# Kernel optimization log

Measured on AMD Instinct MI355X. Metric: run time of the kernel, lower is better.

## Reference

```python
import jax, jax.numpy as jnp
import numpy as np

N, E, IN_DIM, HID = 50000, 800000, 512, 256
EPS = 1e-5


def _gat_layer(x, W, a_src, a_dst, b, src, dst, n, heads, ch):
    # x: [N, F_in] -> h: [N, H, C]
    h = (x @ W).reshape(n, heads, ch)
    alpha_src = jnp.sum(h * a_src, axis=-1)  # [N, H]
    alpha_dst = jnp.sum(h * a_dst, axis=-1)  # [N, H]
    e = jax.nn.leaky_relu(alpha_src[src] + alpha_dst[dst], negative_slope=0.2)  # [E', H]
    # segment softmax over incoming edges of each destination node
    m = jax.ops.segment_max(e, dst, num_segments=n)  # [N, H]
    ex = jnp.exp(e - m[dst])
    den = jax.ops.segment_sum(ex, dst, num_segments=n)  # [N, H]
    alpha = ex / den[dst]
    out = jax.ops.segment_sum(alpha[:, :, None] * h[src], dst, num_segments=n)  # [N, H, C]
    return out.reshape(n, heads * ch) + b


def _layer_norm(x, w, b):
    mu = jnp.mean(x, axis=-1, keepdims=True)
    var = jnp.mean(jnp.square(x - mu), axis=-1, keepdims=True)
    return (x - mu) * jax.lax.rsqrt(var + EPS) * w + b


def setup_inputs() -> dict:
    key = jax.random.key(0)
    ks = jax.random.split(key, 16)
    d = {}
    d['x'] = jax.random.normal(ks[0], (N, IN_DIM), dtype=jnp.float32)
    d['edge_index'] = jax.random.randint(ks[1], (2, E), 0, N, dtype=jnp.int32)
    s = 0.05
    # layer 0: GATConv(512, 64, heads=4)
    d['W0'] = jax.random.normal(ks[2], (IN_DIM, HID), dtype=jnp.float32) * s
    d['as0'] = jax.random.normal(ks[3], (4, 64), dtype=jnp.float32) * s
    d['ad0'] = jax.random.normal(ks[4], (4, 64), dtype=jnp.float32) * s
    d['b0'] = jnp.zeros((HID,), dtype=jnp.float32)
    d['lnw0'] = jnp.ones((HID,), dtype=jnp.float32)
    d['lnb0'] = jnp.zeros((HID,), dtype=jnp.float32)
    # layer 1: GATConv(256, 64, heads=4)
    d['W1'] = jax.random.normal(ks[5], (HID, HID), dtype=jnp.float32) * s
    d['as1'] = jax.random.normal(ks[6], (4, 64), dtype=jnp.float32) * s
    d['ad1'] = jax.random.normal(ks[7], (4, 64), dtype=jnp.float32) * s
    d['b1'] = jnp.zeros((HID,), dtype=jnp.float32)
    d['lnw1'] = jnp.ones((HID,), dtype=jnp.float32)
    d['lnb1'] = jnp.zeros((HID,), dtype=jnp.float32)
    # layer 2: GATConv(256, 256, heads=1)
    d['W2'] = jax.random.normal(ks[8], (HID, HID), dtype=jnp.float32) * s
    d['as2'] = jax.random.normal(ks[9], (1, HID), dtype=jnp.float32) * s
    d['ad2'] = jax.random.normal(ks[10], (1, HID), dtype=jnp.float32) * s
    d['b2'] = jnp.zeros((HID,), dtype=jnp.float32)
    d['lnw2'] = jnp.ones((HID,), dtype=jnp.float32)
    d['lnb2'] = jnp.zeros((HID,), dtype=jnp.float32)
    return d


def reference(x, edge_index, W0, as0, ad0, b0, lnw0, lnb0,
              W1, as1, ad1, b1, lnw1, lnb1,
              W2, as2, ad2, b2, lnw2, lnb2):
    n = x.shape[0]
    loop = jnp.arange(n, dtype=edge_index.dtype)
    src = jnp.concatenate([edge_index[0], loop])  # PyG add_self_loops=True
    dst = jnp.concatenate([edge_index[1], loop])
    h = _gat_layer(x, W0, as0, ad0, b0, src, dst, n, 4, 64)
    h = jax.nn.elu(_layer_norm(h, lnw0, lnb0))
    h = _gat_layer(h, W1, as1, ad1, b1, src, dst, n, 4, 64)
    h = jax.nn.elu(_layer_norm(h, lnw1, lnb1))
    h = _gat_layer(h, W2, as2, ad2, b2, src, dst, n, 1, HID)
    h = jax.nn.elu(_layer_norm(h, lnw2, lnb2))
    return h
```

## Files before the change

kernel.cpp:

```cpp
#include <hip/hip_runtime.h>

#define HID 256
#define EPSV 1e-5f
#define ASTR 72
#define BSTR 40

typedef __bf16 bf16x8 __attribute__((ext_vector_type(8)));
typedef float  floatx4 __attribute__((ext_vector_type(4)));

static __device__ __forceinline__ ushort f2bf(float f) {
  union { float f; unsigned int i; } c; c.f = f;
  unsigned int u = c.i;
  u += 0x7FFFu + ((u >> 16) & 1u);
  return (ushort)(u >> 16);
}
static __device__ __forceinline__ float bf2f(ushort u) {
  union { unsigned int i; float f; } c; c.i = ((unsigned int)u) << 16; return c.f;
}

__global__ void count_kernel(const int* __restrict__ ei, int* __restrict__ deg, int E, int tot) {
  int i = blockIdx.x * blockDim.x + threadIdx.x;
  if (i < tot) {
    int dst = (i < E) ? ei[E + i] : (i - E);
    atomicAdd(&deg[dst], 1);
  }
}

__global__ void scanA_kernel(const int* __restrict__ deg, int* __restrict__ incl,
                             int* __restrict__ sums, int n) {
  __shared__ int buf[1024];
  const int t = threadIdx.x;
  const int i = blockIdx.x * 1024 + t;
  int x = (i < n) ? deg[i] : 0;
  buf[t] = x;
  __syncthreads();
  for (int off = 1; off < 1024; off <<= 1) {
    int v = (t >= off) ? buf[t - off] : 0;
    __syncthreads();
    buf[t] += v;
    __syncthreads();
  }
  if (i < n) incl[i] = buf[t];
  if (t == 1023) sums[blockIdx.x] = buf[1023];
}

__global__ void scanB_kernel(int* __restrict__ sums, int* __restrict__ offs, int nblk) {
  __shared__ int buf[256];
  const int t = threadIdx.x;
  int x = (t < nblk) ? sums[t] : 0;
  buf[t] = x;
  __syncthreads();
  for (int off = 1; off < 256; off <<= 1) {
    int v = (t >= off) ? buf[t - off] : 0;
    __syncthreads();
    buf[t] += v;
    __syncthreads();
  }
  if (t < nblk) offs[t] = buf[t] - x;
  if (t == nblk) offs[nblk] = buf[nblk - 1];
}

__global__ void scanC_kernel(const int* __restrict__ deg, const int* __restrict__ incl,
                             const int* __restrict__ offs, int* __restrict__ rp,
                             int* __restrict__ cur, int n, int nblk) {
  const int i = blockIdx.x * 1024 + threadIdx.x;
  if (i < n) {
    int v = offs[blockIdx.x] + incl[i] - deg[i];
    rp[i] = v;
    cur[i] = v;
  }
  if (i == 0) rp[n] = offs[nblk];
}

__global__ void scatter_kernel(const int* __restrict__ ei, int* __restrict__ cur,
                               int* __restrict__ csr, int E, int tot) {
  int i = blockIdx.x * blockDim.x + threadIdx.x;
  if (i < tot) {
    int src = (i < E) ? ei[i] : (i - E);
    int dst = (i < E) ? ei[E + i] : (i - E);
    int pos = atomicAdd(&cur[dst], 1);
    csr[pos] = src;
  }
}

__global__ __launch_bounds__(256) void transpose_kernel(
    const float* __restrict__ W, ushort* __restrict__ Wt, int K) {
  __shared__ ushort tile[32][33];
  const int tx = threadIdx.x & 31, ty = threadIdx.x >> 5;
  const int bm = blockIdx.x * 32;
  const int bk = blockIdx.y * 32;
  #pragma unroll
  for (int yy = ty; yy < 32; yy += 8)
    tile[tx][yy] = f2bf(W[(size_t)(bk + yy) * 256 + bm + tx]);
  __syncthreads();
  #pragma unroll
  for (int yy = ty; yy < 32; yy += 8)
    Wt[(size_t)(bm + yy) * K + bk + tx] = tile[yy][tx];
}

static __device__ __forceinline__ void alpha_epilogue(
    const floatx4 (&acc)[4][4], const float* __restrict__ avs,
    const float* __restrict__ avd, float* __restrict__ asrc,
    float* __restrict__ adst, int row0, int col0, int wm, int wn,
    int quad, int m16, int nrows) {
  float sv[4], dv[4];
  #pragma unroll
  for (int j = 0; j < 4; j++) {
    int col = col0 + wn + j * 16 + m16;
    sv[j] = avs[col];
    dv[j] = avd[col];
  }
  const int idx = (col0 + wn) >> 6;
  #pragma unroll
  for (int i = 0; i < 4; i++) {
    #pragma unroll
    for (int r = 0; r < 4; r++) {
      int row = row0 + wm + i * 16 + quad * 4 + r;
      float s = 0.f, d = 0.f;
      #pragma unroll
      for (int j = 0; j < 4; j++) {
        s = fmaf(acc[i][j][r], sv[j], s);
        d = fmaf(acc[i][j][r], dv[j], d);
      }
      #pragma unroll
      for (int o = 1; o < 16; o <<= 1) { s += __shfl_xor(s, o); d += __shfl_xor(d, o); }
      if (m16 == 0 && row < nrows) {
        asrc[row * 4 + idx] = s;
        adst[row * 4 + idx] = d;
      }
    }
  }
}

__global__ __launch_bounds__(256) void gemm_kernel(
    const float* __restrict__ A, const ushort* __restrict__ Bt,
    ushort* __restrict__ hb, const float* __restrict__ avs,
    const float* __restrict__ avd, float* __restrict__ asrc,
    float* __restrict__ adst, int nrows, int K) {
  __shared__ ushort At[128 * ASTR];
  __shared__ ushort Bs[128 * BSTR];
  const int tid  = threadIdx.x;
  const int lane = tid & 63;
  const int wave = tid >> 6;
  const int quad = lane >> 4;
  const int m16  = lane & 15;
  const int row0 = blockIdx.x * 128;
  const int col0 = blockIdx.y * 128;
  const int wm = (wave >> 1) * 64;
  const int wn = (wave & 1) * 64;

  floatx4 acc[4][4];
  #pragma unroll
  for (int i = 0; i < 4; i++)
    #pragma unroll
    for (int j = 0; j < 4; j++) acc[i][j] = (floatx4){0.f, 0.f, 0.f, 0.f};

  const int arow = tid >> 3;
  const int acol = (tid & 7) * 4;
  const int brow = tid >> 2;
  const int bcol = (tid & 3) * 8;

  const float* pa[4];
  const ushort* pb[2];
  #pragma unroll
  for (int i = 0; i < 4; i++) {
    int r = arow + 32 * i;
    int ar = min(row0 + r, nrows - 1);
    pa[i] = A + (size_t)ar * K + acol;
  }
  #pragma unroll
  for (int i = 0; i < 2; i++)
    pb[i] = Bt + (size_t)(col0 + brow + 64 * i) * K + bcol;

  floatx4 rA[4];
  int4 rB[2];
  #pragma unroll
  for (int i = 0; i < 4; i++) rA[i] = *(const floatx4*)pa[i];
  #pragma unroll
  for (int i = 0; i < 2; i++) rB[i] = *(const int4*)pb[i];

  for (int k0 = 0; k0 < K; k0 += 32) {
    #pragma unroll
    for (int i = 0; i < 4; i++) {
      int r = arow + 32 * i;
      floatx4 v = rA[i];
      unsigned u0 = __float_as_uint(v[0]), u1 = __float_as_uint(v[1]);
      unsigned u2 = __float_as_uint(v[2]), u3 = __float_as_uint(v[3]);
      unsigned ph0 = __builtin_amdgcn_perm(u1, u0, 0x07060302u);
      unsigned ph1 = __builtin_amdgcn_perm(u3, u2, 0x07060302u);
      float l0 = v[0] - __uint_as_float(u0 & 0xffff0000u);
      float l1 = v[1] - __uint_as_float(u1 & 0xffff0000u);
      float l2 = v[2] - __uint_as_float(u2 & 0xffff0000u);
      float l3 = v[3] - __uint_as_float(u3 & 0xffff0000u);
      unsigned pl0 = __builtin_amdgcn_perm(__float_as_uint(l1), __float_as_uint(l0), 0x07060302u);
      unsigned pl1 = __builtin_amdgcn_perm(__float_as_uint(l3), __float_as_uint(l2), 0x07060302u);
      *(uint2*)&At[r * ASTR + acol]      = make_uint2(ph0, ph1);
      *(uint2*)&At[r * ASTR + 32 + acol] = make_uint2(pl0, pl1);
    }
    #pragma unroll
    for (int i = 0; i < 2; i++)
      *(int4*)&Bs[(brow + 64 * i) * BSTR + bcol] = rB[i];
    __syncthreads();
    if (k0 + 32 < K) {
      #pragma unroll
      for (int i = 0; i < 4; i++) rA[i] = *(const floatx4*)(pa[i] + k0 + 32);
      #pragma unroll
      for (int i = 0; i < 2; i++) rB[i] = *(const int4*)(pb[i] + k0 + 32);
    }
    bf16x8 bfr[4];
    #pragma unroll
    for (int j = 0; j < 4; j++)
      bfr[j] = *(const bf16x8*)&Bs[(wn + j * 16 + m16) * BSTR + quad * 8];
    #pragma unroll
    for (int p = 0; p < 2; p++) {
      bf16x8 af[4];
      #pragma unroll
      for (int i = 0; i < 4; i++)
        af[i] = *(const bf16x8*)&At[(wm + i * 16 + m16) * ASTR + p * 32 + quad * 8];
      #pragma unroll
      for (int i = 0; i < 4; i++)
        #pragma unroll
        for (int j = 0; j < 4; j++)
          acc[i][j] = __builtin_amdgcn_mfma_f32_16x16x32_bf16(af[i], bfr[j], acc[i][j], 0, 0, 0);
    }
    __syncthreads();
  }
  #pragma unroll
  for (int i = 0; i < 4; i++) {
    int rbase = row0 + wm + i * 16 + quad * 4;
    #pragma unroll
    for (int j = 0; j < 4; j++) {
      int col = col0 + wn + j * 16 + m16;
      #pragma unroll
      for (int r = 0; r < 4; r++) {
        int row = rbase + r;
        if (row < nrows) hb[(size_t)row * HID + col] = f2bf(acc[i][j][r]);
      }
    }
  }
  alpha_epilogue(acc, avs, avd, asrc, adst, row0, col0, wm, wn, quad, m16, nrows);
}

__global__ __launch_bounds__(256) void gemm_packed_kernel(
    const ushort* __restrict__ A, const ushort* __restrict__ Bt,
    ushort* __restrict__ hb, const float* __restrict__ avs,
    const float* __restrict__ avd, float* __restrict__ asrc,
    float* __restrict__ adst, int nrows) {
  __shared__ ushort At[128 * BSTR];
  __shared__ ushort Bs[128 * BSTR];
  const int tid  = threadIdx.x;
  const int lane = tid & 63;
  const int wave = tid >> 6;
  const int quad = lane >> 4;
  const int m16  = lane & 15;
  const int row0 = blockIdx.x * 128;
  const int col0 = blockIdx.y * 128;
  const int wm = (wave >> 1) * 64;
  const int wn = (wave & 1) * 64;

  floatx4 acc[4][4];
  #pragma unroll
  for (int i = 0; i < 4; i++)
    #pragma unroll
    for (int j = 0; j < 4; j++) acc[i][j] = (floatx4){0.f, 0.f, 0.f, 0.f};

  const int srow = tid >> 2;
  const int scol = (tid & 3) * 8;

  const ushort* pa[2];
  const ushort* pb[2];
  #pragma unroll
  for (int i = 0; i < 2; i++) {
    int r = srow + 64 * i;
    int ar = min(row0 + r, nrows - 1);
    pa[i] = A + (size_t)ar * 512 + scol;
    pb[i] = Bt + (size_t)(col0 + r) * 256 + scol;
  }

  int4 rA[2], rB[2];
  #pragma unroll
  for (int i = 0; i < 2; i++) { rA[i] = *(const int4*)pa[i]; rB[i] = *(const int4*)pb[i]; }

  for (int k0 = 0; k0 < 512; k0 += 32) {
    #pragma unroll
    for (int i = 0; i < 2; i++) {
      int r = srow + 64 * i;
      *(int4*)&At[r * BSTR + scol] = rA[i];
      *(int4*)&Bs[r * BSTR + scol] = rB[i];
    }
    __syncthreads();
    if (k0 + 32 < 512) {
      int kn = k0 + 32, kbn = kn & 255;
      #pragma unroll
      for (int i = 0; i < 2; i++) {
        rA[i] = *(const int4*)(pa[i] + kn);
        rB[i] = *(const int4*)(pb[i] + kbn);
      }
    }
    bf16x8 af[4], bfr[4];
    #pragma unroll
    for (int j = 0; j < 4; j++)
      bfr[j] = *(const bf16x8*)&Bs[(wn + j * 16 + m16) * BSTR + quad * 8];
    #pragma unroll
    for (int i = 0; i < 4; i++)
      af[i] = *(const bf16x8*)&At[(wm + i * 16 + m16) * BSTR + quad * 8];
    #pragma unroll
    for (int i = 0; i < 4; i++)
      #pragma unroll
      for (int j = 0; j < 4; j++)
        acc[i][j] = __builtin_amdgcn_mfma_f32_16x16x32_bf16(af[i], bfr[j], acc[i][j], 0, 0, 0);
    __syncthreads();
  }
  #pragma unroll
  for (int i = 0; i < 4; i++) {
    int rbase = row0 + wm + i * 16 + quad * 4;
    #pragma unroll
    for (int j = 0; j < 4; j++) {
      int col = col0 + wn + j * 16 + m16;
      #pragma unroll
      for (int r = 0; r < 4; r++) {
        int row = rbase + r;
        if (row < nrows) hb[(size_t)row * HID + col] = f2bf(acc[i][j][r]);
      }
    }
  }
  alpha_epilogue(acc, avs, avd, asrc, adst, row0, col0, wm, wn, quad, m16, nrows);
}

__global__ __launch_bounds__(256) void agg_ln_kernel(
    const ushort* __restrict__ hb, const float* __restrict__ asrc,
    const float* __restrict__ adst, const int* __restrict__ rp,
    const int* __restrict__ csr,
    const float* __restrict__ bias, const float* __restrict__ lnw,
    const float* __restrict__ lnb, ushort* __restrict__ apk,
    float* __restrict__ fout, int H, int n) {
  __shared__ float2 exs[4][64];
  const int t = threadIdx.x;
  const int w = t >> 6, lane = t & 63;
  const int nid = blockIdx.x * 4 + w;
  if (nid >= n) return;
  const int CH = (H == 4) ? 16 : 64;
  const int jj = lane & (CH - 1);
  const int hh = (H == 4) ? (lane >> 4) : 0;
  const int ch = 4 * lane;
  float ad;
  if (H == 4) {
    ad = adst[nid * 4 + hh];
  } else {
    floatx4 t4 = *(const floatx4*)(adst + nid * 4);
    ad = t4[0] + t4[1] + t4[2] + t4[3];
  }
  const int beg = rp[nid], end = rp[nid + 1];
  const char* hbase = (const char*)hb + ch * 2;
  float den = 0.f;
  float a0 = 0.f, a1 = 0.f, a2 = 0.f, a3 = 0.f;
  float b0 = 0.f, b1 = 0.f, b2 = 0.f, b3 = 0.f;
  float c0_ = 0.f, c1 = 0.f, c2 = 0.f, c3 = 0.f;
  float d0_ = 0.f, d1 = 0.f, d2 = 0.f, d3 = 0.f;

  int snext = 0;
  {
    int cnt0 = min(CH, end - beg);
    if (lane < cnt0) snext = csr[beg + lane];
  }

  for (int c0 = beg; c0 < end; c0 += CH) {
    const int cnt = min(CH, end - c0);
    int s = snext;
    const int nc0 = c0 + CH;
    if (nc0 < end) {
      int ncnt = min(CH, end - nc0);
      if (lane < ncnt) snext = csr[nc0 + lane];
    }
    s = __shfl(s, jj);
    float ex = 0.f;
    if (jj < cnt) {
      float e;
      if (H == 4) {
        e = asrc[s * 4 + hh] + ad;
      } else {
        floatx4 t4 = *(const floatx4*)(asrc + s * 4);
        e = t4[0] + t4[1] + t4[2] + t4[3] + ad;
      }
      e = (e > 0.f) ? e : 0.2f * e;
      ex = __expf(fminf(e, 60.f));
    }
    exs[w][lane] = make_float2(ex, __int_as_float(s << 9));
    float dsum = ex;
    #pragma unroll
    for (int o = 32; o > 0; o >>= 1)
      if (o < CH) dsum += __shfl_xor(dsum, o);
    den += dsum;
    const float2* exw = &exs[w][hh * CH];
    int j = 0;
    for (; j + 4 <= cnt; j += 4) {
      float2 q0 = exw[j];
      float2 q1 = exw[j + 1];
      float2 q2 = exw[j + 2];
      float2 q3 = exw[j + 3];
      uint2 u0 = *(const uint2*)(hbase + __float_as_int(q0.y));
      uint2 u1 = *(const uint2*)(hbase + __float_as_int(q1.y));
      uint2 u2 = *(const uint2*)(hbase + __float_as_int(q2.y));
      uint2 u3 = *(const uint2*)(hbase + __float_as_int(q3.y));
      a0 = fmaf(q0.x, __uint_as_float(u0.x << 16), a0);
      a1 = fmaf(q0.x, __uint_as_float(u0.x & 0xffff0000u), a1);
      a2 = fmaf(q0.x, __uint_as_float(u0.y << 16), a2);
      a3 = fmaf(q0.x, __uint_as_float(u0.y & 0xffff0000u), a3);
      b0 = fmaf(q1.x, __uint_as_float(u1.x << 16), b0);
      b1 = fmaf(q1.x, __uint_as_float(u1.x & 0xffff0000u), b1);
      b2 = fmaf(q1.x, __uint_as_float(u1.y << 16), b2);
      b3 = fmaf(q1.x, __uint_as_float(u1.y & 0xffff0000u), b3);
      c0_ = fmaf(q2.x, __uint_as_float(u2.x << 16), c0_);
      c1 = fmaf(q2.x, __uint_as_float(u2.x & 0xffff0000u), c1);
      c2 = fmaf(q2.x, __uint_as_float(u2.y << 16), c2);
      c3 = fmaf(q2.x, __uint_as_float(u2.y & 0xffff0000u), c3);
      d0_ = fmaf(q3.x, __uint_as_float(u3.x << 16), d0_);
      d1 = fmaf(q3.x, __uint_as_float(u3.x & 0xffff0000u), d1);
      d2 = fmaf(q3.x, __uint_as_float(u3.y << 16), d2);
      d3 = fmaf(q3.x, __uint_as_float(u3.y & 0xffff0000u), d3);
    }
    for (; j < cnt; ++j) {
      float2 q0 = exw[j];
      uint2 u0 = *(const uint2*)(hbase + __float_as_int(q0.y));
      a0 = fmaf(q0.x, __uint_as_float(u0.x << 16), a0);
      a1 = fmaf(q0.x, __uint_as_float(u0.x & 0xffff0000u), a1);
      a2 = fmaf(q0.x, __uint_as_float(u0.y << 16), a2);
      a3 = fmaf(q0.x, __uint_as_float(u0.y & 0xffff0000u), a3);
    }
  }
  a0 += b0 + c0_ + d0_;
  a1 += b1 + c1 + d1;
  a2 += b2 + c2 + d2;
  a3 += b3 + c3 + d3;

  const float inv = 1.f / den;
  const floatx4 bia = *(const floatx4*)(bias + ch);
  float v0 = a0 * inv + bia[0];
  float v1 = a1 * inv + bia[1];
  float v2 = a2 * inv + bia[2];
  float v3 = a3 * inv + bia[3];
  float r1 = v0 + v1 + v2 + v3;
  #pragma unroll
  for (int o = 32; o > 0; o >>= 1) r1 += __shfl_xor(r1, o);
  float mu = r1 * (1.f / HID);
  float e0 = v0 - mu, e1 = v1 - mu, e2 = v2 - mu, e3 = v3 - mu;
  float r2 = e0 * e0 + e1 * e1 + e2 * e2 + e3 * e3;
  #pragma unroll
  for (int o = 32; o > 0; o >>= 1) r2 += __shfl_xor(r2, o);
  float rstd = rsqrtf(r2 * (1.f / HID) + EPSV);
  const floatx4 wv = *(const floatx4*)(lnw + ch);
  const floatx4 bv = *(const floatx4*)(lnb + ch);
  float y0 = e0 * rstd * wv[0] + bv[0];
  float y1 = e1 * rstd * wv[1] + bv[1];
  float y2 = e2 * rstd * wv[2] + bv[2];
  float y3 = e3 * rstd * wv[3] + bv[3];
  float o0 = (y0 > 0.f) ? y0 : expm1f(y0);
  float o1 = (y1 > 0.f) ? y1 : expm1f(y1);
  float o2 = (y2 > 0.f) ? y2 : expm1f(y2);
  float o3 = (y3 > 0.f) ? y3 : expm1f(y3);
  if (apk) {
    union { ushort us[4]; unsigned long long u64; } ph, pl;
    ushort h0 = f2bf(o0), h1 = f2bf(o1), h2 = f2bf(o2), h3 = f2bf(o3);
    ph.us[0] = h0; ph.us[1] = h1; ph.us[2] = h2; ph.us[3] = h3;
    pl.us[0] = f2bf(o0 - bf2f(h0)); pl.us[1] = f2bf(o1 - bf2f(h1));
    pl.us[2] = f2bf(o2 - bf2f(h2)); pl.us[3] = f2bf(o3 - bf2f(h3));
    *(unsigned long long*)(apk + (size_t)nid * 512 + ch)       = ph.u64;
    *(unsigned long long*)(apk + (size_t)nid * 512 + 256 + ch) = pl.u64;
  } else {
    floatx4 ov; ov[0] = o0; ov[1] = o1; ov[2] = o2; ov[3] = o3;
    *(floatx4*)(fout + (size_t)nid * HID + ch) = ov;
  }
}

extern "C" void kernel_launch(void* const* d_in, const int* in_sizes, int n_in,
                              void* d_out, int out_size, void* d_ws, size_t ws_size,
                              hipStream_t stream) {
  const float* x  = (const float*)d_in[0];
  const int*   ei = (const int*)d_in[1];
  const float* Wm[3]  = {(const float*)d_in[2], (const float*)d_in[8],  (const float*)d_in[14]};
  const float* Avs[3] = {(const float*)d_in[3], (const float*)d_in[9],  (const float*)d_in[15]};
  const float* Avd[3] = {(const float*)d_in[4], (const float*)d_in[10], (const float*)d_in[16]};
  const float* Bia[3] = {(const float*)d_in[5], (const float*)d_in[11], (const float*)d_in[17]};
  const float* Lnw[3] = {(const float*)d_in[6], (const float*)d_in[12], (const float*)d_in[18]};
  const float* Lnb[3] = {(const float*)d_in[7], (const float*)d_in[13], (const float*)d_in[19]};
  const int n = in_sizes[0] / 512;
  const int E = in_sizes[1] / 2;
  const int tot = E + n;
  const int nblk = (n + 1023) / 1024;

  char* p = (char*)d_ws;
  ushort* hb   = (ushort*)p; p += (size_t)n * HID * 2;
  ushort* apk  = (ushort*)p; p += (size_t)n * 512 * 2;
  ushort* Wt   = (ushort*)p; p += 256 * 512 * 2;
  float*  asrc = (float*)p;  p += (size_t)n * 4 * 4;
  float*  adst = (float*)p;  p += (size_t)n * 4 * 4;
  int* rp   = (int*)p; p += (size_t)(n + 1) * 4;
  int* cur  = (int*)p; p += (size_t)n * 4;
  int* csr  = (int*)p; p += (size_t)tot * 4;
  int* deg  = (int*)p; p += (size_t)n * 4;
  int* incl = (int*)p; p += (size_t)n * 4;
  int* sums = (int*)p; p += (size_t)(nblk + 1) * 4;
  int* offs = (int*)p; p += (size_t)(nblk + 1) * 4;

  hipMemsetAsync(deg, 0, (size_t)n * 4, stream);
  count_kernel<<<(tot + 255) / 256, 256, 0, stream>>>(ei, deg, E, tot);
  scanA_kernel<<<nblk, 1024, 0, stream>>>(deg, incl, sums, n);
  scanB_kernel<<<1, 256, 0, stream>>>(sums, offs, nblk);
  scanC_kernel<<<nblk, 1024, 0, stream>>>(deg, incl, offs, rp, cur, n, nblk);
  scatter_kernel<<<(tot + 255) / 256, 256, 0, stream>>>(ei, cur, csr, E, tot);

  const int KB[3] = {512, 256, 256};
  const int HH[3] = {4, 4, 1};
  dim3 gg((n + 127) / 128, 2);
  for (int l = 0; l < 3; l++) {
    dim3 tg(8, KB[l] / 32);
    transpose_kernel<<<tg, 256, 0, stream>>>(Wm[l], Wt, KB[l]);
    if (l == 0)
      gemm_kernel<<<gg, 256, 0, stream>>>(x, Wt, hb, Avs[l], Avd[l], asrc, adst, n, 512);
    else
      gemm_packed_kernel<<<gg, 256, 0, stream>>>(apk, Wt, hb, Avs[l], Avd[l], asrc, adst, n);
    agg_ln_kernel<<<(n + 3) / 4, 256, 0, stream>>>(
        hb, asrc, adst, rp, csr, Bia[l], Lnw[l], Lnb[l],
        (l < 2) ? apk : (ushort*)nullptr,
        (l == 2) ? (float*)d_out : (float*)nullptr, HH[l], n);
  }
}
```

Before: 747.2 us.

## Double GEMM K-tile to 64 and drop register prefetch pipelining

```diff
diff --git a/kernel.cpp b/kernel.cpp
--- a/kernel.cpp
+++ b/kernel.cpp
@@ -2,8 +2,8 @@
 
 #define HID 256
 #define EPSV 1e-5f
-#define ASTR 72
-#define BSTR 40
+#define ASTR 136
+#define BSTR 72
 
 typedef __bf16 bf16x8 __attribute__((ext_vector_type(8)));
 typedef float  floatx4 __attribute__((ext_vector_type(4)));
@@ -160,68 +160,69 @@
   const int brow = tid >> 2;
   const int bcol = (tid & 3) * 8;
 
-  const float* pa[4];
-  const ushort* pb[2];
-  #pragma unroll
-  for (int i = 0; i < 4; i++) {
-    int r = arow + 32 * i;
-    int ar = min(row0 + r, nrows - 1);
-    pa[i] = A + (size_t)ar * K + acol;
-  }
-  #pragma unroll
-  for (int i = 0; i < 2; i++)
-    pb[i] = Bt + (size_t)(col0 + brow + 64 * i) * K + bcol;
-
-  floatx4 rA[4];
-  int4 rB[2];
-  #pragma unroll
-  for (int i = 0; i < 4; i++) rA[i] = *(const floatx4*)pa[i];
-  #pragma unroll
-  for (int i = 0; i < 2; i++) rB[i] = *(const int4*)pb[i];
-
-  for (int k0 = 0; k0 < K; k0 += 32) {
+  for (int k0 = 0; k0 < K; k0 += 64) {
+    floatx4 va[4][2];
+    int4 vb[2][2];
+    #pragma unroll
+    for (int i = 0; i < 4; i++) {
+      int ar = min(row0 + arow + 32 * i, nrows - 1);
+      #pragma unroll
+      for (int c = 0; c < 2; c++)
+        va[i][c] = *(const floatx4*)(A + (size_t)ar * K + k0 + c * 32 + acol);
+    }
+    #pragma unroll
+    for (int i = 0; i < 2; i++) {
+      int r = brow + 64 * i;
+      #pragma unroll
+      for (int c = 0; c < 2; c++)
+        vb[i][c] = *(const int4*)(Bt + (size_t)(col0 + r) * K + k0 + c * 32 + bcol);
+    }
     #pragma unroll
     for (int i = 0; i < 4; i++) {
       int r = arow + 32 * i;
-      floatx4 v = rA[i];
-      unsigned u0 = __float_as_uint(v[0]), u1 = __float_as_uint(v[1]);
-      unsigned u2 = __float_as_uint(v[2]), u3 = __float_as_uint(v[3]);
-      unsigned ph0 = __builtin_amdgcn_perm(u1, u0, 0x07060302u);
-      unsigned ph1 = __builtin_amdgcn_perm(u3, u2, 0x07060302u);
-      float l0 = v[0] - __uint_as_float(u0 & 0xffff0000u);
-      float l1 = v[1] - __uint_as_float(u1 & 0xffff0000u);
-      float l2 = v[2] - __uint_as_float(u2 & 0xffff0000u);
-      float l3 = v[3] - __uint_as_float(u3 & 0xffff0000u);
-      unsigned pl0 = __builtin_amdgcn_perm(__float_as_uint(l1), __float_as_uint(l0), 0x07060302u);
-      unsigned pl1 = __builtin_amdgcn_perm(__float_as_uint(l3), __float_as_uint(l2), 0x07060302u);
-      *(uint2*)&At[r * ASTR + acol]      = make_uint2(ph0, ph1);
-      *(uint2*)&At[r * ASTR + 32 + acol] = make_uint2(pl0, pl1);
-    }
-    #pragma unroll
-    for (int i = 0; i < 2; i++)
-      *(int4*)&Bs[(brow + 64 * i) * BSTR + bcol] = rB[i];
-    __syncthreads();
-    if (k0 + 32 < K) {
-      #pragma unroll
-      for (int i = 0; i < 4; i++) rA[i] = *(const floatx4*)(pa[i] + k0 + 32);
-      #pragma unroll
-      for (int i = 0; i < 2; i++) rB[i] = *(const int4*)(pb[i] + k0 + 32);
-    }
-    bf16x8 bfr[4];
-    #pragma unroll
-    for (int j = 0; j < 4; j++)
-      bfr[j] = *(const bf16x8*)&Bs[(wn + j * 16 + m16) * BSTR + quad * 8];
-    #pragma unroll
-    for (int p = 0; p < 2; p++) {
-      bf16x8 af[4];
-      #pragma unroll
-      for (int i = 0; i < 4; i++)
-        af[i] = *(const bf16x8*)&At[(wm + i * 16 + m16) * ASTR + p * 32 + quad * 8];
-      #pragma unroll
-      for (int i = 0; i < 4; i++)
+      #pragma unroll
+      for (int c = 0; c < 2; c++) {
+        floatx4 v = va[i][c];
+        unsigned u0 = __float_as_uint(v[0]), u1 = __float_as_uint(v[1]);
+        unsigned u2 = __float_as_uint(v[2]), u3 = __float_as_uint(v[3]);
+        unsigned ph0 = __builtin_amdgcn_perm(u1, u0, 0x07060302u);
+        unsigned ph1 = __builtin_amdgcn_perm(u3, u2, 0x07060302u);
+        float l0 = v[0] - __uint_as_float(u0 & 0xffff0000u);
+        float l1 = v[1] - __uint_as_float(u1 & 0xffff0000u);
+        float l2 = v[2] - __uint_as_float(u2 & 0xffff0000u);
+        float l3 = v[3] - __uint_as_float(u3 & 0xffff0000u);
+        unsigned pl0 = __builtin_amdgcn_perm(__float_as_uint(l1), __float_as_uint(l0), 0x07060302u);
+        unsigned pl1 = __builtin_amdgcn_perm(__float_as_uint(l3), __float_as_uint(l2), 0x07060302u);
+        *(uint2*)&At[r * ASTR + c * 32 + acol]      = make_uint2(ph0, ph1);
+        *(uint2*)&At[r * ASTR + 64 + c * 32 + acol] = make_uint2(pl0, pl1);
+      }
+    }
+    #pragma unroll
+    for (int i = 0; i < 2; i++) {
+      int r = brow + 64 * i;
+      #pragma unroll
+      for (int c = 0; c < 2; c++)
+        *(int4*)&Bs[r * BSTR + c * 32 + bcol] = vb[i][c];
+    }
+    __syncthreads();
+    #pragma unroll
+    for (int kk = 0; kk < 2; kk++) {
+      bf16x8 bfr[4];
+      #pragma unroll
+      for (int j = 0; j < 4; j++)
+        bfr[j] = *(const bf16x8*)&Bs[(wn + j * 16 + m16) * BSTR + kk * 32 + quad * 8];
+      #pragma unroll
+      for (int p = 0; p < 2; p++) {
+        bf16x8 af[4];
         #pragma unroll
-        for (int j = 0; j < 4; j++)
-          acc[i][j] = __builtin_amdgcn_mfma_f32_16x16x32_bf16(af[i], bfr[j], acc[i][j], 0, 0, 0);
+        for (int i = 0; i < 4; i++)
+          af[i] = *(const bf16x8*)&At[(wm + i * 16 + m16) * ASTR + p * 64 + kk * 32 + quad * 8];
+        #pragma unroll
+        for (int i = 0; i < 4; i++)
+          #pragma unroll
+          for (int j = 0; j < 4; j++)
+            acc[i][j] = __builtin_amdgcn_mfma_f32_16x16x32_bf16(af[i], bfr[j], acc[i][j], 0, 0, 0);
+      }
     }
     __syncthreads();
   }
@@ -267,48 +268,44 @@
   const int srow = tid >> 2;
   const int scol = (tid & 3) * 8;
 
-  const ushort* pa[2];
-  const ushort* pb[2];
-  #pragma unroll
-  for (int i = 0; i < 2; i++) {
-    int r = srow + 64 * i;
-    int ar = min(row0 + r, nrows - 1);
-    pa[i] = A + (size_t)ar * 512 + scol;
-    pb[i] = Bt + (size_t)(col0 + r) * 256 + scol;
-  }
-
-  int4 rA[2], rB[2];
-  #pragma unroll
-  for (int i = 0; i < 2; i++) { rA[i] = *(const int4*)pa[i]; rB[i] = *(const int4*)pb[i]; }
-
-  for (int k0 = 0; k0 < 512; k0 += 32) {
+  for (int k0 = 0; k0 < 512; k0 += 64) {
+    const int kb = k0 & 255;
+    int4 va[2][2], vb[2][2];
     #pragma unroll
     for (int i = 0; i < 2; i++) {
       int r = srow + 64 * i;
-      *(int4*)&At[r * BSTR + scol] = rA[i];
-      *(int4*)&Bs[r * BSTR + scol] = rB[i];
-    }
-    __syncthreads();
-    if (k0 + 32 < 512) {
-      int kn = k0 + 32, kbn = kn & 255;
-      #pragma unroll
-      for (int i = 0; i < 2; i++) {
-        rA[i] = *(const int4*)(pa[i] + kn);
-        rB[i] = *(const int4*)(pb[i] + kbn);
-      }
-    }
-    bf16x8 af[4], bfr[4];
-    #pragma unroll
-    for (int j = 0; j < 4; j++)
-      bfr[j] = *(const bf16x8*)&Bs[(wn + j * 16 + m16) * BSTR + quad * 8];
-    #pragma unroll
-    for (int i = 0; i < 4; i++)
-      af[i] = *(const bf16x8*)&At[(wm + i * 16 + m16) * BSTR + quad * 8];
-    #pragma unroll
-    for (int i = 0; i < 4; i++)
+      int ar = min(row0 + r, nrows - 1);
+      #pragma unroll
+      for (int c = 0; c < 2; c++) {
+        va[i][c] = *(const int4*)(A + (size_t)ar * 512 + k0 + c * 32 + scol);
+        vb[i][c] = *(const int4*)(Bt + (size_t)(col0 + r) * 256 + kb + c * 32 + scol);
+      }
+    }
+    #pragma unroll
+    for (int i = 0; i < 2; i++) {
+      int r = srow + 64 * i;
+      #pragma unroll
+      for (int c = 0; c < 2; c++) {
+        *(int4*)&At[r * BSTR + c * 32 + scol] = va[i][c];
+        *(int4*)&Bs[r * BSTR + c * 32 + scol] = vb[i][c];
+      }
+    }
+    __syncthreads();
+    #pragma unroll
+    for (int kk = 0; kk < 2; kk++) {
+      bf16x8 af[4], bfr[4];
       #pragma unroll
       for (int j = 0; j < 4; j++)
-        acc[i][j] = __builtin_amdgcn_mfma_f32_16x16x32_bf16(af[i], bfr[j], acc[i][j], 0, 0, 0);
+        bfr[j] = *(const bf16x8*)&Bs[(wn + j * 16 + m16) * BSTR + kk * 32 + quad * 8];
+      #pragma unroll
+      for (int i = 0; i < 4; i++)
+        af[i] = *(const bf16x8*)&At[(wm + i * 16 + m16) * BSTR + kk * 32 + quad * 8];
+      #pragma unroll
+      for (int i = 0; i < 4; i++)
+        #pragma unroll
+        for (int j = 0; j < 4; j++)
+          acc[i][j] = __builtin_amdgcn_mfma_f32_16x16x32_bf16(af[i], bfr[j], acc[i][j], 0, 0, 0);
+    }
     __syncthreads();
   }
   #pragma unroll
```

New measurement: 617.3 us. 17.4% less time.
